# Kernel tuning notes

Measured on AMD Instinct MI355X. Metric: run time of the kernel, lower is better.

The kernel has to match this reference:

```python
import jax, jax.numpy as jnp
import numpy as np

DIM = 128
EXPAND = 2
INTERNAL = DIM * EXPAND  # 256
MAX_SEQ = 2048
BATCH = 32
GATE_DECAY = 3.0


def _gated_cell(x, Wa, ba, Wi, bi, g):
    # x: [B,S,D]; Wa,Wi: [E,D]; ba,bi,g: [E]
    pa = jnp.einsum('bsd,ed->bse', x, Wa) + ba          # projected activation
    pi = jnp.einsum('bsd,ed->bse', x, Wi) + bi          # projected input
    reset_gate = jax.nn.sigmoid(pa)
    input_gate = jax.nn.sigmoid(pi)
    alpha = jax.nn.sigmoid(g)                           # [E]
    a = alpha / jnp.power(GATE_DECAY, reset_gate)       # adaptive alpha [B,S,E]
    u = jnp.sqrt(1.0 - a * a) * (input_gate * pi)       # per-step input [B,S,E]

    def step(h, au):
        a_t, u_t = au
        h = a_t * h + u_t
        return h, h

    h0 = jnp.zeros((x.shape[0], Wa.shape[0]), x.dtype)
    _, ys = jax.lax.scan(step, h0, (a.transpose(1, 0, 2), u.transpose(1, 0, 2)))
    return ys.transpose(1, 0, 2)                        # [B,S,E]


def _recency_weights(seq_len, dtype):
    w = jnp.exp(jnp.linspace(0.0, 3.0, MAX_SEQ))[:seq_len]
    return w.astype(dtype).reshape(1, -1, 1)


def setup_inputs() -> dict:
    key = jax.random.key(0)
    ks = jax.random.split(key, 12)
    std = 1.0 / np.sqrt(DIM)  # kaiming fan_in linear
    lo = float(np.log(0.9 / 0.1))
    hi = float(np.log(0.999 / 0.001))
    d = {
        'x': jax.random.normal(ks[0], (BATCH, MAX_SEQ, DIM), jnp.float32),
        'Wa_u': jax.random.normal(ks[1], (INTERNAL, DIM), jnp.float32) * std,
        'ba_u': jnp.zeros((INTERNAL,), jnp.float32),
        'Wi_u': jax.random.normal(ks[2], (INTERNAL, DIM), jnp.float32) * std,
        'bi_u': jnp.zeros((INTERNAL,), jnp.float32),
        'g_u': jax.random.uniform(ks[3], (INTERNAL,), jnp.float32, lo, hi),
        'Wa_w': jax.random.normal(ks[4], (INTERNAL, DIM), jnp.float32) * std,
        'ba_w': jnp.zeros((INTERNAL,), jnp.float32),
        'Wi_w': jax.random.normal(ks[5], (INTERNAL, DIM), jnp.float32) * std,
        'bi_w': jnp.zeros((INTERNAL,), jnp.float32),
        'g_w': jax.random.uniform(ks[6], (INTERNAL,), jnp.float32, lo, hi),
        'Wf': jax.random.normal(ks[7], (DIM, 4 * DIM), jnp.float32) * (1.0 / np.sqrt(4 * DIM)),
        'bf': jnp.zeros((DIM,), jnp.float32),
    }
    return d


def reference(x, Wa_u, ba_u, Wi_u, bi_u, g_u, Wa_w, ba_w, Wi_w, bi_w, g_w, Wf, bf):
    unweighted = _gated_cell(x, Wa_u, ba_u, Wi_u, bi_u, g_u)          # [B,S,2D]
    xw = x * _recency_weights(x.shape[1], x.dtype)
    weighted = _gated_cell(xw, Wa_w, ba_w, Wi_w, bi_w, g_w)           # [B,S,2D]
    combined = jnp.concatenate([unweighted, weighted], axis=-1)       # [B,S,4D]
    return jnp.einsum('bsf,df->bsd', combined, Wf) + bf               # [B,S,D]
```

## Files before the change

kernel.cpp:

```cpp
#include <hip/hip_runtime.h>
#include <hip/hip_fp16.h>
#include <cstddef>
#include <cstdint>

#define DIM 128
#define SEQ 2048
#define NB 32
#define NCH 512
#define NROWS (NB * SEQ)

typedef _Float16 half8 __attribute__((ext_vector_type(8)));
typedef float    f32x4 __attribute__((ext_vector_type(4)));

#define CMB_BYTES ((size_t)NROWS * NCH * 2)
#define WFG_OFF   CMB_BYTES
#define WFG_BYTES ((size_t)NCH * DIM * 2)
#define WS_NEEDED (WFG_OFF + WFG_BYTES)

__device__ __forceinline__ float sigf(float v) {
    return __builtin_amdgcn_rcpf(1.0f + __builtin_amdgcn_exp2f(v * -1.44269504f));
}

__device__ __forceinline__ half8 cvt8(float4 v0, float4 v1) {
    auto p0 = __builtin_amdgcn_cvt_pkrtz(v0.x, v0.y);
    auto p1 = __builtin_amdgcn_cvt_pkrtz(v0.z, v0.w);
    auto p2 = __builtin_amdgcn_cvt_pkrtz(v1.x, v1.y);
    auto p3 = __builtin_amdgcn_cvt_pkrtz(v1.z, v1.w);
    union U { half8 h8; decltype(p0) p[4]; } u;
    u.p[0] = p0; u.p[1] = p1; u.p[2] = p2; u.p[3] = p3;
    return u.h8;
}

__device__ __forceinline__ void gload_lds16(const _Float16* g, _Float16* l) {
    __builtin_amdgcn_global_load_lds(
        (const __attribute__((address_space(1))) void*)g,
        (__attribute__((address_space(3))) void*)l,
        16, 0, 0);
}

__global__ __launch_bounds__(512, 2) void kfused(
        const float* __restrict__ x,
        const float* __restrict__ Wa_u, const float* __restrict__ ba_u,
        const float* __restrict__ Wi_u, const float* __restrict__ bi_u,
        const float* __restrict__ g_u,
        const float* __restrict__ Wa_w, const float* __restrict__ ba_w,
        const float* __restrict__ Wi_w, const float* __restrict__ bi_w,
        const float* __restrict__ g_w,
        const float* __restrict__ Wf, _Float16* __restrict__ Wfg,
        _Float16* __restrict__ cmb) {
    __shared__ _Float16 Bs[8192];
    __shared__ float2   Wseg[2][8][33];
    __shared__ float    carryL[2][32];

    const int tid  = threadIdx.x;
    const int lane = tid & 63;
    const int w    = tid >> 6;
    const int quad = lane >> 4;
    const int n16  = lane & 15;

    const int b  = blockIdx.x;
    const int cg = blockIdx.y;
    const int p  = cg >> 3;
    const int ebase = (cg & 7) * 32;

    if (b == 0) {
        int tg = cg * 512 + tid;
#pragma unroll
        for (int i = 0; i < 8; ++i) {
            int o = tg * 8 + i;
            int j    = o & 7;
            int l2   = (o >> 3) & 63;
            int q2   = l2 >> 4, m16 = l2 & 15;
            int ct   = (o >> 9) & 7;
            int ks2  = (o >> 12) & 1;
            int kb2  = o >> 13;
            int k = kb2 * 64 + ks2 * 32 + q2 * 8 + j;
            int n = ct * 16 + m16;
            Wfg[o] = (_Float16)Wf[n * NCH + k];
        }
    }

    const float* Wa  = p ? Wa_w : Wa_u;
    const float* Wi  = p ? Wi_w : Wi_u;
    const float* bap = p ? ba_w : ba_u;
    const float* bip = p ? bi_w : bi_u;
    const float* gp  = p ? g_w  : g_u;

    for (int sl = tid; sl < 1024; sl += 512) {
        int l  = sl & 63;
        int nt = (sl >> 6) & 3;
        int ks = sl >> 8;
        int qq = l >> 4, nn = l & 15;
        int e = ebase + (nt & 1) * 16 + nn;
        const float* Wp = (nt >> 1) ? Wi : Wa;
        const float* src = Wp + (size_t)e * DIM + ks * 32 + qq * 8;
        float4 v0 = *(const float4*)src;
        float4 v1 = *(const float4*)(src + 4);
        *(half8*)&Bs[sl * 8] = cvt8(v0, v1);
    }

    const float NL2E = -1.44269504f;
    float rba[2], rbi[2], ral[2], rba2[2];
#pragma unroll
    for (int hh = 0; hh < 2; ++hh) {
        int e = ebase + hh * 16 + n16;
        rba[hh] = bap[e];
        rbi[hh] = bip[e];
        ral[hh] = sigf(gp[e]);
        rba2[hh] = rba[hh] * NL2E;
    }
    if (tid < 32) carryL[0][tid] = 0.0f;

    float scb = __expf((float)(w * 16 + quad * 4) * (3.0f / 2047.0f));
    const float r1    = __expf(3.0f / 2047.0f);
    const float r2    = r1 * r1;
    const float r3    = r2 * r1;
    const float cs128 = __expf(128.0f * 3.0f / 2047.0f);

    const float* xbase = x + ((size_t)b * SEQ + (size_t)(w * 16 + n16)) * DIM + quad * 8;
    _Float16* dst0 = cmb + (size_t)(cg >> 1) * 8192 + (size_t)w * 1024
                   + (size_t)(cg & 1) * 512
                   + (size_t)quad * 32 + (size_t)(n16 >> 3) * 128 + (n16 & 7);

    __syncthreads();

    half8 bfr[8];
#pragma unroll
    for (int ks = 0; ks < 2; ++ks)
#pragma unroll
        for (int nt = 0; nt < 4; ++nt)
            bfr[ks * 4 + nt] = *(const half8*)&Bs[(ks * 256 + nt * 64 + lane) * 8];

    half8 af[4];
    {
        float4 xf0[8];
#pragma unroll
        for (int ks = 0; ks < 4; ++ks) {
            xf0[2 * ks]     = *(const float4*)(xbase + ks * 32);
            xf0[2 * ks + 1] = *(const float4*)(xbase + ks * 32 + 4);
        }
#pragma unroll
        for (int ks = 0; ks < 4; ++ks)
            af[ks] = cvt8(xf0[2 * ks], xf0[2 * ks + 1]);
    }

    for (int t = 0; t < 16; ++t) {
        f32x4 acc[4];
#pragma unroll
        for (int nt = 0; nt < 4; ++nt) acc[nt] = (f32x4){0.f, 0.f, 0.f, 0.f};
#pragma unroll
        for (int ks = 0; ks < 4; ++ks) {
            half8 a = af[ks];
#pragma unroll
            for (int nt = 0; nt < 4; ++nt) {
                half8 bb = (ks < 2)
                    ? bfr[ks * 4 + nt]
                    : *(const half8*)&Bs[(ks * 256 + nt * 64 + lane) * 8];
                acc[nt] = __builtin_amdgcn_mfma_f32_16x16x32_f16(a, bb, acc[nt], 0, 0, 0);
            }
        }

        const float* ab = xbase + (size_t)((t + 1) & 15) * 128 * DIM;
        float4 xf1[4];
#pragma unroll
        for (int ks = 0; ks < 2; ++ks) {
            xf1[2 * ks]     = *(const float4*)(ab + ks * 32);
            xf1[2 * ks + 1] = *(const float4*)(ab + ks * 32 + 4);
        }

        float sc[4], sc2[4];
        if (p) { sc[0] = scb; sc[1] = scb * r1; sc[2] = scb * r2; sc[3] = scb * r3; }
        else   { sc[0] = sc[1] = sc[2] = sc[3] = 1.0f; }
        scb *= cs128;
#pragma unroll
        for (int reg = 0; reg < 4; ++reg) sc2[reg] = sc[reg] * NL2E;

        float a_s[2][4], u_s[2][4];
        float IA[2], IU[2], EA[2], EU[2];
#pragma unroll
        for (int hh = 0; hh < 2; ++hh) {
            float A4 = 1.0f, U4 = 0.0f;
#pragma unroll
            for (int reg = 0; reg < 4; ++reg) {
                float pi  = fmaf(acc[2 + hh][reg], sc[reg], rbi[hh]);
                float ea  = __builtin_amdgcn_exp2f(fmaf(acc[hh][reg], sc2[reg], rba2[hh]));
                float rst = __builtin_amdgcn_rcpf(1.0f + ea);
                float ig  = sigf(pi);
                float a   = ral[hh] * __builtin_amdgcn_exp2f(-rst * 1.5849625007211562f);
                float m   = fmaxf(fmaf(-a, a, 1.0f), 0.0f);
                float u   = __builtin_amdgcn_sqrtf(m) * (ig * pi);
                a_s[hh][reg] = a; u_s[hh][reg] = u;
                A4 *= a;
                U4 = fmaf(a, U4, u);
            }
            float A = A4, U = U4;
            float Ap = __shfl_up(A, 16); float Up = __shfl_up(U, 16);
            bool c1 = quad >= 1;
            U = c1 ? fmaf(A, Up, U) : U;
            A = c1 ? A * Ap : A;
            Ap = __shfl_up(A, 32); Up = __shfl_up(U, 32);
            bool c2 = quad >= 2;
            U = c2 ? fmaf(A, Up, U) : U;
            A = c2 ? A * Ap : A;
            IA[hh] = A; IU[hh] = U;
            float Ae = __shfl_up(A, 16), Ue = __shfl_up(U, 16);
            EA[hh] = (quad == 0) ? 1.0f : Ae;
            EU[hh] = (quad == 0) ? 0.0f : Ue;
        }
        if (quad == 3) {
#pragma unroll
            for (int hh = 0; hh < 2; ++hh)
                Wseg[t & 1][w][hh * 16 + n16] = make_float2(IA[hh], IU[hh]);
        }

        __syncthreads();

        float4 xf2[4];
#pragma unroll
        for (int ks = 0; ks < 2; ++ks) {
            xf2[2 * ks]     = *(const float4*)(ab + 64 + ks * 32);
            xf2[2 * ks + 1] = *(const float4*)(ab + 64 + ks * 32 + 4);
        }
        af[0] = cvt8(xf1[0], xf1[1]);
        af[1] = cvt8(xf1[2], xf1[3]);

        _Float16* dstT = dst0 + (size_t)((b * 16 + t) * 8) * 8192;
#pragma unroll
        for (int hh = 0; hh < 2; ++hh) {
            int ch = hh * 16 + n16;
            float h = carryL[t & 1][ch];
            float2 wv[7];
#pragma unroll
            for (int jj = 0; jj < 7; ++jj)
                wv[jj] = Wseg[t & 1][jj][ch];
#pragma unroll
            for (int jj = 0; jj < 7; ++jj)
                if (jj < w) h = fmaf(wv[jj].x, h, wv[jj].y);
            h = fmaf(EA[hh], h, EU[hh]);
#pragma unroll
            for (int reg = 0; reg < 4; ++reg) {
                h = fmaf(a_s[hh][reg], h, u_s[hh][reg]);
                dstT[hh * 256 + reg * 8] = (_Float16)h;
            }
            if (w == 7 && quad == 3)
                carryL[(t + 1) & 1][ch] = h;
        }

        af[2] = cvt8(xf2[0], xf2[1]);
        af[3] = cvt8(xf2[2], xf2[3]);
    }
}

__global__ __launch_bounds__(256, 2) void k3_mfma(
        const _Float16* __restrict__ cmbF, const _Float16* __restrict__ Wfg,
        const float* __restrict__ bfv, float* __restrict__ out) {
    __shared__ _Float16 As[2][8192];
    __shared__ _Float16 Bs[2][8192];

    const int tid  = threadIdx.x;
    const int lane = tid & 63;
    const int w    = tid >> 6;
    const int rb   = blockIdx.x;
    const int row0 = rb * 128;
    const int q    = lane >> 4;
    const int nn   = lane & 15;

    f32x4 acc[2][8];
#pragma unroll
    for (int rt = 0; rt < 2; ++rt)
#pragma unroll
        for (int ct = 0; ct < 8; ++ct)
            acc[rt][ct] = (f32x4){0.0f, 0.0f, 0.0f, 0.0f};

#define K3_STAGE(buf, kb)                                                     \
    {                                                                         \
        const _Float16* sa = cmbF + ((size_t)rb * 8 + (kb)) * 8192            \
                           + (size_t)w * 2048 + (size_t)lane * 8;             \
        const _Float16* sb = Wfg + (size_t)(kb) * 8192                        \
                           + (size_t)w * 2048 + (size_t)lane * 8;             \
        _Float16* la = &As[buf][w * 2048];                                    \
        _Float16* lb = &Bs[buf][w * 2048];                                    \
        _Pragma("unroll")                                                     \
        for (int i = 0; i < 4; ++i) {                                         \
            gload_lds16(sa + i * 512, la + i * 512);                          \
            gload_lds16(sb + i * 512, lb + i * 512);                          \
        }                                                                     \
    }

    K3_STAGE(0, 0);
    __syncthreads();

    for (int kb = 0; kb < 8; ++kb) {
        const int cur = kb & 1;
        if (kb < 7) K3_STAGE(cur ^ 1, kb + 1);

#pragma unroll
        for (int ks = 0; ks < 2; ++ks) {
            half8 a0 = *(const half8*)&As[cur][(((w * 2 + 0) * 2 + ks) * 512) + lane * 8];
            half8 a1 = *(const half8*)&As[cur][(((w * 2 + 1) * 2 + ks) * 512) + lane * 8];
#pragma unroll
            for (int ct = 0; ct < 8; ++ct) {
                half8 bb = *(const half8*)&Bs[cur][((ks * 8 + ct) * 512) + lane * 8];
                acc[0][ct] = __builtin_amdgcn_mfma_f32_16x16x32_f16(a0, bb, acc[0][ct], 0, 0, 0);
                acc[1][ct] = __builtin_amdgcn_mfma_f32_16x16x32_f16(a1, bb, acc[1][ct], 0, 0, 0);
            }
        }
        __syncthreads();
    }

#pragma unroll
    for (int rt = 0; rt < 2; ++rt) {
        int rbase = row0 + w * 32 + rt * 16 + q * 4;
#pragma unroll
        for (int ct = 0; ct < 8; ++ct) {
            int col = ct * 16 + nn;
            float bias = bfv[col];
#pragma unroll
            for (int reg = 0; reg < 4; ++reg)
                out[(size_t)(rbase + reg) * DIM + col] = acc[rt][ct][reg] + bias;
        }
    }
#undef K3_STAGE
}

extern "C" void kernel_launch(void* const* d_in, const int* in_sizes, int n_in,
                              void* d_out, int out_size, void* d_ws, size_t ws_size,
                              hipStream_t stream) {
    if (ws_size < WS_NEEDED) return;

    const float* x    = (const float*)d_in[0];
    const float* Wa_u = (const float*)d_in[1];
    const float* ba_u = (const float*)d_in[2];
    const float* Wi_u = (const float*)d_in[3];
    const float* bi_u = (const float*)d_in[4];
    const float* g_u  = (const float*)d_in[5];
    const float* Wa_w = (const float*)d_in[6];
    const float* ba_w = (const float*)d_in[7];
    const float* Wi_w = (const float*)d_in[8];
    const float* bi_w = (const float*)d_in[9];
    const float* g_w  = (const float*)d_in[10];
    const float* Wf   = (const float*)d_in[11];
    const float* bfv  = (const float*)d_in[12];
    float* out = (float*)d_out;

    char* ws = (char*)d_ws;
    _Float16* cmb = (_Float16*)ws;
    _Float16* Wfg = (_Float16*)(ws + WFG_OFF);

    hipLaunchKernelGGL(kfused, dim3(32, 16), dim3(512), 0, stream,
                       x, Wa_u, ba_u, Wi_u, bi_u, g_u,
                       Wa_w, ba_w, Wi_w, bi_w, g_w, Wf, Wfg, cmb);
    hipLaunchKernelGGL(k3_mfma, dim3(512), dim3(256), 0, stream,
                       cmb, Wfg, bfv, out);
}
```

Measured before the change: 186.1 us.

## Merge scan and output GEMM into one persistent kernel with grid barrier

Folds the gated-scan kernel and the final MFMA projection kernel into a single launch of 512 blocks. An atomic-counter grid barrier in workspace separates the two phases, and each block then computes a 128-row output tile with 8 waves of 16 rows each. This removes the second kernel launch and the gap between kernels. In exchange it adds a memset, a spin barrier that assumes all 512 blocks are co-resident, and a 64KB shared buffer that may limit occupancy.

Result: slower. 433.9 us (+133.2%).

```diff
diff --git a/kernel.cpp b/kernel.cpp
--- a/kernel.cpp
+++ b/kernel.cpp
@@ -15,7 +15,8 @@
 #define CMB_BYTES ((size_t)NROWS * NCH * 2)
 #define WFG_OFF   CMB_BYTES
 #define WFG_BYTES ((size_t)NCH * DIM * 2)
-#define WS_NEEDED (WFG_OFF + WFG_BYTES)
+#define BAR_OFF   (WFG_OFF + WFG_BYTES)
+#define WS_NEEDED (BAR_OFF + 64)
 
 __device__ __forceinline__ float sigf(float v) {
     return __builtin_amdgcn_rcpf(1.0f + __builtin_amdgcn_exp2f(v * -1.44269504f));
@@ -38,7 +39,7 @@
         16, 0, 0);
 }
 
-__global__ __launch_bounds__(512, 2) void kfused(
+__global__ __launch_bounds__(512, 2) void kmega(
         const float* __restrict__ x,
         const float* __restrict__ Wa_u, const float* __restrict__ ba_u,
         const float* __restrict__ Wi_u, const float* __restrict__ bi_u,
@@ -46,11 +47,14 @@
         const float* __restrict__ Wa_w, const float* __restrict__ ba_w,
         const float* __restrict__ Wi_w, const float* __restrict__ bi_w,
         const float* __restrict__ g_w,
-        const float* __restrict__ Wf, _Float16* __restrict__ Wfg,
-        _Float16* __restrict__ cmb) {
-    __shared__ _Float16 Bs[8192];
-    __shared__ float2   Wseg[2][8][33];
-    __shared__ float    carryL[2][32];
+        const float* __restrict__ Wf, const float* __restrict__ bfv,
+        _Float16* __restrict__ Wfg, _Float16* __restrict__ cmb,
+        float* __restrict__ out, unsigned* __restrict__ bar) {
+    __shared__ __align__(16) char smem[65536];
+
+    _Float16* Bs    = (_Float16*)smem;
+    float2*   wseg  = (float2*)(smem + 16384);
+    float*    carry = (float*)(smem + 16384 + 4224);
 
     const int tid  = threadIdx.x;
     const int lane = tid & 63;
@@ -58,8 +62,9 @@
     const int quad = lane >> 4;
     const int n16  = lane & 15;
 
-    const int b  = blockIdx.x;
-    const int cg = blockIdx.y;
+    const int id = blockIdx.x;
+    const int b  = id & 31;
+    const int cg = id >> 5;
     const int p  = cg >> 3;
     const int ebase = (cg & 7) * 32;
 
@@ -109,7 +114,7 @@
         ral[hh] = sigf(gp[e]);
         rba2[hh] = rba[hh] * NL2E;
     }
-    if (tid < 32) carryL[0][tid] = 0.0f;
+    if (tid < 32) carry[tid] = 0.0f;
 
     float scb = __expf((float)(w * 16 + quad * 4) * (3.0f / 2047.0f));
     const float r1    = __expf(3.0f / 2047.0f);
@@ -210,7 +215,7 @@
         if (quad == 3) {
 #pragma unroll
             for (int hh = 0; hh < 2; ++hh)
-                Wseg[t & 1][w][hh * 16 + n16] = make_float2(IA[hh], IU[hh]);
+                wseg[((t & 1) * 8 + w) * 33 + hh * 16 + n16] = make_float2(IA[hh], IU[hh]);
         }
 
         __syncthreads();
@@ -228,11 +233,11 @@
 #pragma unroll
         for (int hh = 0; hh < 2; ++hh) {
             int ch = hh * 16 + n16;
-            float h = carryL[t & 1][ch];
+            float h = carry[(t & 1) * 32 + ch];
             float2 wv[7];
 #pragma unroll
             for (int jj = 0; jj < 7; ++jj)
-                wv[jj] = Wseg[t & 1][jj][ch];
+                wv[jj] = wseg[((t & 1) * 8 + jj) * 33 + ch];
 #pragma unroll
             for (int jj = 0; jj < 7; ++jj)
                 if (jj < w) h = fmaf(wv[jj].x, h, wv[jj].y);
@@ -243,84 +248,80 @@
                 dstT[hh * 256 + reg * 8] = (_Float16)h;
             }
             if (w == 7 && quad == 3)
-                carryL[(t + 1) & 1][ch] = h;
+                carry[((t + 1) & 1) * 32 + ch] = h;
         }
 
         af[2] = cvt8(xf2[0], xf2[1]);
         af[3] = cvt8(xf2[2], xf2[3]);
     }
-}
-
-__global__ __launch_bounds__(256, 2) void k3_mfma(
-        const _Float16* __restrict__ cmbF, const _Float16* __restrict__ Wfg,
-        const float* __restrict__ bfv, float* __restrict__ out) {
-    __shared__ _Float16 As[2][8192];
-    __shared__ _Float16 Bs[2][8192];
-
-    const int tid  = threadIdx.x;
-    const int lane = tid & 63;
-    const int w    = tid >> 6;
-    const int rb   = blockIdx.x;
-    const int row0 = rb * 128;
-    const int q    = lane >> 4;
-    const int nn   = lane & 15;
-
-    f32x4 acc[2][8];
-#pragma unroll
-    for (int rt = 0; rt < 2; ++rt)
-#pragma unroll
-        for (int ct = 0; ct < 8; ++ct)
-            acc[rt][ct] = (f32x4){0.0f, 0.0f, 0.0f, 0.0f};
-
-#define K3_STAGE(buf, kb)                                                     \
-    {                                                                         \
-        const _Float16* sa = cmbF + ((size_t)rb * 8 + (kb)) * 8192            \
-                           + (size_t)w * 2048 + (size_t)lane * 8;             \
-        const _Float16* sb = Wfg + (size_t)(kb) * 8192                        \
-                           + (size_t)w * 2048 + (size_t)lane * 8;             \
-        _Float16* la = &As[buf][w * 2048];                                    \
-        _Float16* lb = &Bs[buf][w * 2048];                                    \
-        _Pragma("unroll")                                                     \
-        for (int i = 0; i < 4; ++i) {                                         \
-            gload_lds16(sa + i * 512, la + i * 512);                          \
-            gload_lds16(sb + i * 512, lb + i * 512);                          \
-        }                                                                     \
-    }
-
-    K3_STAGE(0, 0);
+
     __syncthreads();
-
-    for (int kb = 0; kb < 8; ++kb) {
-        const int cur = kb & 1;
-        if (kb < 7) K3_STAGE(cur ^ 1, kb + 1);
-
-#pragma unroll
-        for (int ks = 0; ks < 2; ++ks) {
-            half8 a0 = *(const half8*)&As[cur][(((w * 2 + 0) * 2 + ks) * 512) + lane * 8];
-            half8 a1 = *(const half8*)&As[cur][(((w * 2 + 1) * 2 + ks) * 512) + lane * 8];
-#pragma unroll
-            for (int ct = 0; ct < 8; ++ct) {
-                half8 bb = *(const half8*)&Bs[cur][((ks * 8 + ct) * 512) + lane * 8];
-                acc[0][ct] = __builtin_amdgcn_mfma_f32_16x16x32_f16(a0, bb, acc[0][ct], 0, 0, 0);
-                acc[1][ct] = __builtin_amdgcn_mfma_f32_16x16x32_f16(a1, bb, acc[1][ct], 0, 0, 0);
+    __threadfence();
+    if (tid == 0) {
+        __hip_atomic_fetch_add(bar, 1u, __ATOMIC_ACQ_REL, __HIP_MEMORY_SCOPE_AGENT);
+        unsigned v;
+        do {
+            __builtin_amdgcn_s_sleep(8);
+            v = __hip_atomic_load(bar, __ATOMIC_ACQUIRE, __HIP_MEMORY_SCOPE_AGENT);
+        } while (v < 512u);
+    }
+    __syncthreads();
+    __threadfence();
+
+    {
+        _Float16* AsB = (_Float16*)smem;
+        _Float16* BsB = (_Float16*)(smem + 32768);
+        const int rb   = id;
+        const int row0 = rb * 128;
+        const int q    = quad;
+        const int nn   = n16;
+
+        f32x4 acc2[8];
+#pragma unroll
+        for (int ct = 0; ct < 8; ++ct) acc2[ct] = (f32x4){0.f, 0.f, 0.f, 0.f};
+
+#define MSTAGE(buf, kb)                                                       \
+        {                                                                     \
+            const _Float16* sa = cmb + ((size_t)rb * 8 + (kb)) * 8192         \
+                               + (size_t)w * 1024 + (size_t)lane * 8;         \
+            const _Float16* sb = Wfg + (size_t)(kb) * 8192                    \
+                               + (size_t)w * 1024 + (size_t)lane * 8;         \
+            _Float16* la = AsB + (buf) * 8192 + w * 1024;                     \
+            _Float16* lb = BsB + (buf) * 8192 + w * 1024;                     \
+            gload_lds16(sa, la);       gload_lds16(sa + 512, la + 512);       \
+            gload_lds16(sb, lb);       gload_lds16(sb + 512, lb + 512);       \
+        }
+
+        MSTAGE(0, 0);
+        __syncthreads();
+
+        for (int kb = 0; kb < 8; ++kb) {
+            const int cur = kb & 1;
+            if (kb < 7) MSTAGE(cur ^ 1, kb + 1);
+
+#pragma unroll
+            for (int ks = 0; ks < 2; ++ks) {
+                half8 a = *(const half8*)&AsB[cur * 8192 + (w * 2 + ks) * 512 + lane * 8];
+#pragma unroll
+                for (int ct = 0; ct < 8; ++ct) {
+                    half8 bb = *(const half8*)&BsB[cur * 8192 + (ks * 8 + ct) * 512 + lane * 8];
+                    acc2[ct] = __builtin_amdgcn_mfma_f32_16x16x32_f16(a, bb, acc2[ct], 0, 0, 0);
+                }
             }
-        }
-        __syncthreads();
-    }
-
-#pragma unroll
-    for (int rt = 0; rt < 2; ++rt) {
-        int rbase = row0 + w * 32 + rt * 16 + q * 4;
+            __syncthreads();
+        }
+
+        const int rbase = row0 + w * 16 + q * 4;
 #pragma unroll
         for (int ct = 0; ct < 8; ++ct) {
             int col = ct * 16 + nn;
             float bias = bfv[col];
 #pragma unroll
             for (int reg = 0; reg < 4; ++reg)
-                out[(size_t)(rbase + reg) * DIM + col] = acc[rt][ct][reg] + bias;
-        }
-    }
-#undef K3_STAGE
+                out[(size_t)(rbase + reg) * DIM + col] = acc2[ct][reg] + bias;
+        }
+#undef MSTAGE
+    }
 }
 
 extern "C" void kernel_launch(void* const* d_in, const int* in_sizes, int n_in,
@@ -346,10 +347,11 @@
     char* ws = (char*)d_ws;
     _Float16* cmb = (_Float16*)ws;
     _Float16* Wfg = (_Float16*)(ws + WFG_OFF);
-
-    hipLaunchKernelGGL(kfused, dim3(32, 16), dim3(512), 0, stream,
+    unsigned* bar = (unsigned*)(ws + BAR_OFF);
+
+    hipMemsetAsync(bar, 0, 8, stream);
+    hipLaunchKernelGGL(kmega, dim3(512), dim3(512), 0, stream,
                        x, Wa_u, ba_u, Wi_u, bi_u, g_u,
-                       Wa_w, ba_w, Wi_w, bi_w, g_w, Wf, Wfg, cmb);
-    hipLaunchKernelGGL(k3_mfma, dim3(512), dim3(256), 0, stream,
-                       cmb, Wfg, bfv, out);
-}
+                       Wa_w, ba_w, Wi_w, bi_w, g_w,
+                       Wf, bfv, Wfg, cmb, out, bar);
+}
```

## Split k3 GEMM row tiles across two blocks and read Wf directly from global

Applied to the files above, without the earlier changes.

The final projection kernel now launches twice as many blocks, each handling 64 rows (one 16-row MFMA tile per wave) instead of 128. The B operand (fp16 Wf) is no longer staged in LDS and is read straight from global/L2 per wave, which halves LDS use and permits higher occupancy (launch bounds 4). The trade is more redundant global reads of Wf and less register reuse of each B fragment. The first kernel is unchanged and likely dominates total time.

After: 206.8 us. 1.11x slower.

```diff
diff --git a/kernel.cpp b/kernel.cpp
--- a/kernel.cpp
+++ b/kernel.cpp
@@ -251,40 +251,32 @@
     }
 }
 
-__global__ __launch_bounds__(256, 2) void k3_mfma(
+__global__ __launch_bounds__(256, 4) void k3_mfma(
         const _Float16* __restrict__ cmbF, const _Float16* __restrict__ Wfg,
         const float* __restrict__ bfv, float* __restrict__ out) {
-    __shared__ _Float16 As[2][8192];
-    __shared__ _Float16 Bs[2][8192];
+    __shared__ _Float16 As[2][4096];
 
     const int tid  = threadIdx.x;
     const int lane = tid & 63;
     const int w    = tid >> 6;
-    const int rb   = blockIdx.x;
-    const int row0 = rb * 128;
+    const int id   = blockIdx.x;
+    const int rb   = id >> 1;
+    const int half = id & 1;
+    const int rt7  = half * 4 + w;
     const int q    = lane >> 4;
     const int nn   = lane & 15;
 
-    f32x4 acc[2][8];
-#pragma unroll
-    for (int rt = 0; rt < 2; ++rt)
-#pragma unroll
-        for (int ct = 0; ct < 8; ++ct)
-            acc[rt][ct] = (f32x4){0.0f, 0.0f, 0.0f, 0.0f};
+    f32x4 acc[8];
+#pragma unroll
+    for (int ct = 0; ct < 8; ++ct) acc[ct] = (f32x4){0.0f, 0.0f, 0.0f, 0.0f};
 
 #define K3_STAGE(buf, kb)                                                     \
     {                                                                         \
         const _Float16* sa = cmbF + ((size_t)rb * 8 + (kb)) * 8192            \
-                           + (size_t)w * 2048 + (size_t)lane * 8;             \
-        const _Float16* sb = Wfg + (size_t)(kb) * 8192                        \
-                           + (size_t)w * 2048 + (size_t)lane * 8;             \
-        _Float16* la = &As[buf][w * 2048];                                    \
-        _Float16* lb = &Bs[buf][w * 2048];                                    \
-        _Pragma("unroll")                                                     \
-        for (int i = 0; i < 4; ++i) {                                         \
-            gload_lds16(sa + i * 512, la + i * 512);                          \
-            gload_lds16(sb + i * 512, lb + i * 512);                          \
-        }                                                                     \
+                           + (size_t)rt7 * 1024 + (size_t)lane * 8;           \
+        _Float16* la = &As[buf][w * 1024];                                    \
+        gload_lds16(sa, la);                                                  \
+        gload_lds16(sa + 512, la + 512);                                      \
     }
 
     K3_STAGE(0, 0);
@@ -294,31 +286,27 @@
         const int cur = kb & 1;
         if (kb < 7) K3_STAGE(cur ^ 1, kb + 1);
 
+        const _Float16* bsrc = Wfg + (size_t)kb * 8192 + (size_t)lane * 8;
 #pragma unroll
         for (int ks = 0; ks < 2; ++ks) {
-            half8 a0 = *(const half8*)&As[cur][(((w * 2 + 0) * 2 + ks) * 512) + lane * 8];
-            half8 a1 = *(const half8*)&As[cur][(((w * 2 + 1) * 2 + ks) * 512) + lane * 8];
+            half8 a = *(const half8*)&As[cur][w * 1024 + ks * 512 + lane * 8];
 #pragma unroll
             for (int ct = 0; ct < 8; ++ct) {
-                half8 bb = *(const half8*)&Bs[cur][((ks * 8 + ct) * 512) + lane * 8];
-                acc[0][ct] = __builtin_amdgcn_mfma_f32_16x16x32_f16(a0, bb, acc[0][ct], 0, 0, 0);
-                acc[1][ct] = __builtin_amdgcn_mfma_f32_16x16x32_f16(a1, bb, acc[1][ct], 0, 0, 0);
+                half8 bb = *(const half8*)(bsrc + (size_t)(ks * 8 + ct) * 512);
+                acc[ct] = __builtin_amdgcn_mfma_f32_16x16x32_f16(a, bb, acc[ct], 0, 0, 0);
             }
         }
         __syncthreads();
     }
 
-#pragma unroll
-    for (int rt = 0; rt < 2; ++rt) {
-        int rbase = row0 + w * 32 + rt * 16 + q * 4;
-#pragma unroll
-        for (int ct = 0; ct < 8; ++ct) {
-            int col = ct * 16 + nn;
-            float bias = bfv[col];
-#pragma unroll
-            for (int reg = 0; reg < 4; ++reg)
-                out[(size_t)(rbase + reg) * DIM + col] = acc[rt][ct][reg] + bias;
-        }
+    const int rbase = rb * 128 + rt7 * 16 + q * 4;
+#pragma unroll
+    for (int ct = 0; ct < 8; ++ct) {
+        int col = ct * 16 + nn;
+        float bias = bfv[col];
+#pragma unroll
+        for (int reg = 0; reg < 4; ++reg)
+            out[(size_t)(rbase + reg) * DIM + col] = acc[ct][reg] + bias;
     }
 #undef K3_STAGE
 }
@@ -350,6 +338,6 @@
     hipLaunchKernelGGL(kfused, dim3(32, 16), dim3(512), 0, stream,
                        x, Wa_u, ba_u, Wi_u, bi_u, g_u,
                        Wa_w, ba_w, Wi_w, bi_w, g_w, Wf, Wfg, cmb);
-    hipLaunchKernelGGL(k3_mfma, dim3(512), dim3(256), 0, stream,
+    hipLaunchKernelGGL(k3_mfma, dim3(1024), dim3(256), 0, stream,
                        cmb, Wfg, bfv, out);
 }
```
